# Optimization experiments

Measured on AMD Instinct MI355X. Metric: run time of the kernel, lower is better.

## Reference

```python
import jax, jax.numpy as jnp
import numpy as np

N, E, IN, H, C, G = 50000, 1600000, 128, 4, 32, 64  # nodes, edges, in_ch, heads, hidden, graphs
OUT = 1
NEG_SLOPE = 0.2


def setup_inputs() -> dict:
    key = jax.random.key(0)
    ks = jax.random.split(key, 16)
    d = {
        "x": jax.random.normal(ks[0], (N, IN), dtype=jnp.float32),
        "edge_index": jax.random.randint(ks[1], (2, E), 0, N, dtype=jnp.int64),
        "batch": jnp.sort(jax.random.randint(ks[2], (N,), 0, G, dtype=jnp.int64)),
    }
    s = 1.0 / np.sqrt(IN)
    # layer 0: in=IN, layer 1: in=H*C (=128)
    d["W0"] = jax.random.normal(ks[3], (IN, H * C), dtype=jnp.float32) * s
    d["a_src0"] = jax.random.normal(ks[4], (H, C), dtype=jnp.float32) * s
    d["a_dst0"] = jax.random.normal(ks[5], (H, C), dtype=jnp.float32) * s
    d["b0"] = jnp.zeros((H * C,), dtype=jnp.float32)
    d["W1"] = jax.random.normal(ks[6], (H * C, H * C), dtype=jnp.float32) * s
    d["a_src1"] = jax.random.normal(ks[7], (H, C), dtype=jnp.float32) * s
    d["a_dst1"] = jax.random.normal(ks[8], (H, C), dtype=jnp.float32) * s
    d["b1"] = jnp.zeros((H * C,), dtype=jnp.float32)
    d["lin_w"] = jax.random.normal(ks[9], (H * C, OUT), dtype=jnp.float32) * s
    d["lin_b"] = jnp.zeros((OUT,), dtype=jnp.float32)
    return d


def gat_conv(x, src, dst, W, a_src, a_dst, b):
    # x: [N, F_in]; src/dst: [E'] (self-loops already appended, PyG default)
    n = x.shape[0]
    xw = (x @ W).reshape(n, H, C)                      # [N, H, C]
    alpha_s = jnp.sum(xw * a_src, axis=-1)             # [N, H]
    alpha_d = jnp.sum(xw * a_dst, axis=-1)             # [N, H]
    e = jax.nn.leaky_relu(alpha_s[src] + alpha_d[dst], NEG_SLOPE)  # [E', H]
    # segment softmax over edges grouped by destination node
    m = jax.ops.segment_max(e, dst, num_segments=n)    # [N, H]
    ex = jnp.exp(e - m[dst])
    denom = jax.ops.segment_sum(ex, dst, num_segments=n)
    alpha = ex / denom[dst]                            # [E', H]
    msg = xw[src] * alpha[:, :, None]                  # [E', H, C]
    out = jax.ops.segment_sum(msg, dst, num_segments=n)
    return out.reshape(n, H * C) + b


def reference(x, edge_index, batch, W0, a_src0, a_dst0, b0, W1, a_src1, a_dst1, b1, lin_w, lin_b):
    loop = jnp.arange(N, dtype=edge_index.dtype)
    src = jnp.concatenate([edge_index[0], loop])
    dst = jnp.concatenate([edge_index[1], loop])
    h = gat_conv(x.astype(jnp.float32), src, dst, W0, a_src0, a_dst0, b0)
    h = jax.nn.elu(h)  # dropout is identity in eval mode
    h = gat_conv(h, src, dst, W1, a_src1, a_dst1, b1)
    h = jax.nn.elu(h)
    # global_mean_pool
    sums = jax.ops.segment_sum(h, batch, num_segments=G)          # [G, H*C]
    cnts = jax.ops.segment_sum(jnp.ones((N,), h.dtype), batch, num_segments=G)
    pooled = sums / jnp.maximum(cnts, 1.0)[:, None]
    return (pooled @ lin_w + lin_b).squeeze()                     # [G]
```

## Files before the change

kernel.cpp:

```cpp
#include <hip/hip_runtime.h>
#include <hip/hip_bf16.h>

#define NN 50000
#define EE 1600000
#define NEDGE (EE + NN)
#define HH 4
#define HC 128
#define GG 64
#define GMT 64
#define NBKT 196
#define BCAP 12544
#define BKE 2048
#define NB1 ((EE + BKE - 1) / BKE)

__device__ __forceinline__ float lrelu(float x) { return fmaxf(x, 0.2f * x); }

__device__ __forceinline__ unsigned packbf2(float a, float b) {
    unsigned ua = __float_as_uint(a);
    ua = (ua + 0x7fffu + ((ua >> 16) & 1u)) >> 16;
    unsigned ub = __float_as_uint(b);
    ub = (ub + 0x7fffu + ((ub >> 16) & 1u)) >> 16;
    return ua | (ub << 16);
}

__global__ __launch_bounds__(256) void binit(int* __restrict__ bcur) {
    int t = blockIdx.x * 256 + threadIdx.x;
    if (t < NBKT) bcur[t] = t * BCAP;
}

__global__ __launch_bounds__(256) void bucketize(const int* __restrict__ ei,
                                                 int* __restrict__ bcur,
                                                 uint2* __restrict__ pairs) {
    __shared__ int cnt[NBKT], off[NBKT], gbase[NBKT];
    __shared__ int wsum[4], woff[4];
    __shared__ uint2 stage[BKE];
    int t = threadIdx.x;
    int e0 = blockIdx.x * BKE;
    int n = EE - e0; if (n > BKE) n = BKE;
    for (int i = t; i < NBKT; i += 256) cnt[i] = 0;
    __syncthreads();
    unsigned dv[8], sv[8];
    int rk[8];
#pragma unroll
    for (int k = 0; k < 8; ++k) {
        int i = t + k * 256;
        if (i < n) {
            dv[k] = (unsigned)ei[EE + e0 + i];
            sv[k] = (unsigned)ei[e0 + i];
            rk[k] = atomicAdd(&cnt[dv[k] >> 8], 1);
        }
    }
    __syncthreads();
    {
        int v = (t < NBKT) ? cnt[t] : 0;
        int lane = t & 63, wv = t >> 6;
        int x = v;
#pragma unroll
        for (int o = 1; o < 64; o <<= 1) { int y = __shfl_up(x, o); if (lane >= o) x += y; }
        if (lane == 63) wsum[wv] = x;
        __syncthreads();
        if (t == 0) { int r = 0; for (int k2 = 0; k2 < 4; ++k2) { woff[k2] = r; r += wsum[k2]; } }
        __syncthreads();
        if (t < NBKT) off[t] = x - v + woff[wv];
    }
    __syncthreads();
#pragma unroll
    for (int k = 0; k < 8; ++k) {
        int i = t + k * 256;
        if (i < n) stage[off[dv[k] >> 8] + rk[k]] = make_uint2(dv[k], sv[k]);
    }
    __syncthreads();
    if (t < NBKT) { int c = cnt[t]; gbase[t] = c ? atomicAdd(&bcur[t], c) : 0; }
    __syncthreads();
    for (int i = t; i < n; i += 256) {
        uint2 pr = stage[i];
        int b = (int)(pr.x >> 8);
        pairs[(size_t)gbase[b] + (i - off[b])] = pr;
    }
}

__global__ __launch_bounds__(256) void bscan(const int* __restrict__ bcur,
                                             int* __restrict__ bbase) {
    int t = threadIdx.x;
    int v = 0;
    if (t < NBKT) {
        int pcnt = bcur[t] - t * BCAP;
        int nodes = NN - t * 256; if (nodes > 256) nodes = 256;
        v = pcnt + nodes;
    }
    int lane = t & 63, wv = t >> 6;
    int x = v;
#pragma unroll
    for (int o = 1; o < 64; o <<= 1) { int y = __shfl_up(x, o); if (lane >= o) x += y; }
    __shared__ int wsum[4], woff[4];
    if (lane == 63) wsum[wv] = x;
    __syncthreads();
    if (t == 0) { int r = 0; for (int k = 0; k < 4; ++k) { woff[k] = r; r += wsum[k]; } }
    __syncthreads();
    if (t < NBKT) bbase[t] = x - v + woff[wv];
}

__global__ __launch_bounds__(512) void debucket(const uint2* __restrict__ pairs,
                                                const int* __restrict__ bcur,
                                                const int* __restrict__ bbase,
                                                int* __restrict__ row_start,
                                                int* __restrict__ esrc) {
    __shared__ int cnt[256], off[256], cur[256];
    __shared__ int wsum[4], woff[4];
    __shared__ int stage[BCAP + 256];
    int b = blockIdx.x, t = threadIdx.x;
    int n0 = b * 256;
    int nnode = NN - n0; if (nnode > 256) nnode = 256;
    int pcnt = bcur[b] - b * BCAP;
    int base = bbase[b];
    if (t < 256) cnt[t] = 0;
    __syncthreads();
    for (int i = t; i < pcnt; i += 512)
        atomicAdd(&cnt[pairs[(size_t)b * BCAP + i].x & 255u], 1);
    __syncthreads();
    {
        int v = 0, x = 0;
        int lane = t & 63, wv = t >> 6;
        if (t < 256) {
            v = cnt[t] + (t < nnode ? 1 : 0);
            x = v;
#pragma unroll
            for (int o = 1; o < 64; o <<= 1) { int y = __shfl_up(x, o); if (lane >= o) x += y; }
            if (lane == 63) wsum[wv] = x;
        }
        __syncthreads();
        if (t == 0) { int r = 0; for (int k = 0; k < 4; ++k) { woff[k] = r; r += wsum[k]; } }
        __syncthreads();
        if (t < 256) off[t] = x - v + woff[wv];
    }
    __syncthreads();
    if (t < nnode) {
        int o = off[t];
        stage[o] = n0 + t;
        cur[t] = o + 1;
        row_start[n0 + t] = base + o;
    }
    __syncthreads();
    for (int i = t; i < pcnt; i += 512) {
        uint2 pr = pairs[(size_t)b * BCAP + i];
        int p = atomicAdd(&cur[pr.x & 255u], 1);
        stage[p] = (int)pr.y;
    }
    __syncthreads();
    int tot = pcnt + nnode;
    for (int i = t; i < tot; i += 512) esrc[base + i] = stage[i];
    if (b == NBKT - 1 && t == 0) row_start[NN] = NEDGE;
}

__global__ __launch_bounds__(256) void gemm_alpha(
    const float* __restrict__ X, const float* __restrict__ W,
    const float* __restrict__ a_src, const float* __restrict__ a_dst,
    unsigned* __restrict__ xwb, float* __restrict__ as_, float* __restrict__ ad_) {
    __shared__ float xs[GMT][HC + 4];
    int tid = threadIdx.x;
    int n0 = blockIdx.x * GMT;
    for (int i = tid; i < GMT * (HC / 4); i += 256) {
        int r = i >> 5, c4 = i & 31;
        int n = n0 + r;
        float4 v = (n < NN) ? ((const float4*)X)[(size_t)n * 32 + c4]
                            : make_float4(0.f, 0.f, 0.f, 0.f);
        *(float4*)&xs[r][c4 * 4] = v;
    }
    __syncthreads();

    int jg = tid & 31;
    int ng = tid >> 5;
    float4 acc[8] = {};
    for (int k = 0; k < HC; k += 4) {
        float4 wr[4];
#pragma unroll
        for (int dk = 0; dk < 4; ++dk) wr[dk] = ((const float4*)W)[(k + dk) * 32 + jg];
#pragma unroll
        for (int r = 0; r < 8; ++r) {
            float4 xv = *(const float4*)&xs[ng * 8 + r][k];
            acc[r].x = fmaf(xv.x, wr[0].x, acc[r].x);
            acc[r].y = fmaf(xv.x, wr[0].y, acc[r].y);
            acc[r].z = fmaf(xv.x, wr[0].z, acc[r].z);
            acc[r].w = fmaf(xv.x, wr[0].w, acc[r].w);
            acc[r].x = fmaf(xv.y, wr[1].x, acc[r].x);
            acc[r].y = fmaf(xv.y, wr[1].y, acc[r].y);
            acc[r].z = fmaf(xv.y, wr[1].z, acc[r].z);
            acc[r].w = fmaf(xv.y, wr[1].w, acc[r].w);
            acc[r].x = fmaf(xv.z, wr[2].x, acc[r].x);
            acc[r].y = fmaf(xv.z, wr[2].y, acc[r].y);
            acc[r].z = fmaf(xv.z, wr[2].z, acc[r].z);
            acc[r].w = fmaf(xv.z, wr[2].w, acc[r].w);
            acc[r].x = fmaf(xv.w, wr[3].x, acc[r].x);
            acc[r].y = fmaf(xv.w, wr[3].y, acc[r].y);
            acc[r].z = fmaf(xv.w, wr[3].z, acc[r].z);
            acc[r].w = fmaf(xv.w, wr[3].w, acc[r].w);
        }
    }
    float4 asv = ((const float4*)a_src)[jg];
    float4 adv = ((const float4*)a_dst)[jg];
#pragma unroll
    for (int r = 0; r < 8; ++r) {
        int n = n0 + ng * 8 + r;
        float ps = acc[r].x * asv.x + acc[r].y * asv.y + acc[r].z * asv.z + acc[r].w * asv.w;
        float pd = acc[r].x * adv.x + acc[r].y * adv.y + acc[r].z * adv.z + acc[r].w * adv.w;
        ps += __shfl_xor(ps, 1); pd += __shfl_xor(pd, 1);
        ps += __shfl_xor(ps, 2); pd += __shfl_xor(pd, 2);
        ps += __shfl_xor(ps, 4); pd += __shfl_xor(pd, 4);
        if (n < NN) {
            ((uint2*)xwb)[(size_t)n * 32 + jg] =
                make_uint2(packbf2(acc[r].x, acc[r].y), packbf2(acc[r].z, acc[r].w));
            if ((jg & 7) == 0) {
                int h = jg >> 3;
                as_[n * HH + h] = ps;
                ad_[n * HH + h] = pd;
            }
        }
    }
}

#define SWSTR 66
__global__ __launch_bounds__(256) void aggregate(
    const int* __restrict__ esrc, const int* __restrict__ row_start,
    const float* __restrict__ as_, const float* __restrict__ ad_,
    const unsigned* __restrict__ xwb, const float* __restrict__ bias,
    float* __restrict__ out) {
    __shared__ float2 sw_all[4][4 * SWSTR];
    int wid = (int)(threadIdx.x >> 6);
    int node = blockIdx.x * 4 + wid;
    if (node >= NN) return;
    int lane = threadIdx.x & 63;
    float2* sw = &sw_all[wid][0];
    int beg = row_start[node];
    int end = row_start[node + 1];
    float4 ad = ((const float4*)ad_)[node];

    int sub = lane >> 4;
    int c8 = lane & 15;
    int h = c8 >> 2;
    const char* xwp = (const char*)xwb + (c8 << 4);
    const char* asp = (const char*)as_;
    float4 accA = make_float4(0.f, 0.f, 0.f, 0.f);
    float4 accB = make_float4(0.f, 0.f, 0.f, 0.f);
    float dloc = 0.f;

    for (int base = beg; base < end; base += 64) {
        int i = base + lane;
        int cnt = end - base; if (cnt > 64) cnt = 64;
        if (i < end) {
            int s = esrc[i];
            float4 av = *(const float4*)(asp + ((unsigned)s << 4));
            float w0 = __expf(lrelu(av.x + ad.x));
            float w1 = __expf(lrelu(av.y + ad.y));
            float w2 = __expf(lrelu(av.z + ad.z));
            float w3 = __expf(lrelu(av.w + ad.w));
            float sf = __int_as_float(s);
            sw[0 * SWSTR + lane] = make_float2(sf, w0);
            sw[1 * SWSTR + lane] = make_float2(sf, w1);
            sw[2 * SWSTR + lane] = make_float2(sf, w2);
            sw[3 * SWSTR + lane] = make_float2(sf, w3);
        }
        int iters = (cnt + 3) >> 2;
        bool ok = sub < cnt;
        float2 sv = sw[h * SWSTR + (ok ? sub : 0)];
        float wj = ok ? sv.y : 0.f;
        unsigned row = ok ? ((unsigned)__float_as_int(sv.x) << 8) : 0u;
        uint4 v = *(const uint4*)(xwp + row);
        for (int it = 1; it <= iters; ++it) {
            int j1 = (it << 2) + sub;
            bool ok1 = j1 < cnt;
            float2 sv1 = sw[h * SWSTR + (ok1 ? j1 : 0)];
            float w1 = ok1 ? sv1.y : 0.f;
            unsigned row1 = ok1 ? ((unsigned)__float_as_int(sv1.x) << 8) : 0u;
            uint4 v1 = *(const uint4*)(xwp + row1);
            dloc += wj;
            accA.x = fmaf(wj, __uint_as_float(v.x << 16), accA.x);
            accA.y = fmaf(wj, __uint_as_float(v.x & 0xffff0000u), accA.y);
            accA.z = fmaf(wj, __uint_as_float(v.y << 16), accA.z);
            accA.w = fmaf(wj, __uint_as_float(v.y & 0xffff0000u), accA.w);
            accB.x = fmaf(wj, __uint_as_float(v.z << 16), accB.x);
            accB.y = fmaf(wj, __uint_as_float(v.z & 0xffff0000u), accB.y);
            accB.z = fmaf(wj, __uint_as_float(v.w << 16), accB.z);
            accB.w = fmaf(wj, __uint_as_float(v.w & 0xffff0000u), accB.w);
            v = v1; wj = w1;
        }
    }
#pragma unroll
    for (int off = 16; off <= 32; off <<= 1) {
        accA.x += __shfl_xor(accA.x, off);
        accA.y += __shfl_xor(accA.y, off);
        accA.z += __shfl_xor(accA.z, off);
        accA.w += __shfl_xor(accA.w, off);
        accB.x += __shfl_xor(accB.x, off);
        accB.y += __shfl_xor(accB.y, off);
        accB.z += __shfl_xor(accB.z, off);
        accB.w += __shfl_xor(accB.w, off);
        dloc += __shfl_xor(dloc, off);
    }
    if (sub == 0) {
        float inv = 1.f / dloc;
        float4 bb0 = ((const float4*)bias)[c8 * 2];
        float4 bb1 = ((const float4*)bias)[c8 * 2 + 1];
        float4 oA, oB;
        oA.x = fmaf(accA.x, inv, bb0.x);
        oA.y = fmaf(accA.y, inv, bb0.y);
        oA.z = fmaf(accA.z, inv, bb0.z);
        oA.w = fmaf(accA.w, inv, bb0.w);
        oB.x = fmaf(accB.x, inv, bb1.x);
        oB.y = fmaf(accB.y, inv, bb1.y);
        oB.z = fmaf(accB.z, inv, bb1.z);
        oB.w = fmaf(accB.w, inv, bb1.w);
        oA.x = oA.x > 0.f ? oA.x : expm1f(oA.x);
        oA.y = oA.y > 0.f ? oA.y : expm1f(oA.y);
        oA.z = oA.z > 0.f ? oA.z : expm1f(oA.z);
        oA.w = oA.w > 0.f ? oA.w : expm1f(oA.w);
        oB.x = oB.x > 0.f ? oB.x : expm1f(oB.x);
        oB.y = oB.y > 0.f ? oB.y : expm1f(oB.y);
        oB.z = oB.z > 0.f ? oB.z : expm1f(oB.z);
        oB.w = oB.w > 0.f ? oB.w : expm1f(oB.w);
        ((float4*)out)[(size_t)node * 32 + c8 * 2] = oA;
        ((float4*)out)[(size_t)node * 32 + c8 * 2 + 1] = oB;
    }
}

__global__ __launch_bounds__(128) void pool(
    const float* __restrict__ h1, const int* __restrict__ batch,
    float* __restrict__ sums, float* __restrict__ cnts) {
    int j = threadIdx.x;
    int n0 = blockIdx.x * 64;
    int n1 = n0 + 64; if (n1 > NN) n1 = NN;
    if (n0 >= NN) return;
    int cur = batch[n0];
    float local = 0.f;
    int cnt = 0;
    for (int n = n0; n < n1; ++n) {
        int g = batch[n];
        if (g != cur) {
            atomicAdd(&sums[cur * HC + j], local);
            if (j == 0) atomicAdd(&cnts[cur], (float)cnt);
            local = 0.f; cnt = 0; cur = g;
        }
        local += h1[(size_t)n * HC + j];
        ++cnt;
    }
    atomicAdd(&sums[cur * HC + j], local);
    if (j == 0) atomicAdd(&cnts[cur], (float)cnt);
}

__global__ __launch_bounds__(128) void head_out(
    const float* __restrict__ sums, const float* __restrict__ cnts,
    const float* __restrict__ lin_w, const float* __restrict__ lin_b,
    float* __restrict__ out) {
    int g = blockIdx.x;
    int j = threadIdx.x;
    float c = cnts[g];
    c = c > 1.f ? c : 1.f;
    float v = sums[g * HC + j] / c * lin_w[j];
    __shared__ float red[HC];
    red[j] = v;
    __syncthreads();
    for (int off = 64; off > 0; off >>= 1) {
        if (j < off) red[j] += red[j + off];
        __syncthreads();
    }
    if (j == 0) out[g] = red[0] + lin_b[0];
}

extern "C" void kernel_launch(void* const* d_in, const int* in_sizes, int n_in,
                              void* d_out, int out_size, void* d_ws, size_t ws_size,
                              hipStream_t stream) {
    const float* x   = (const float*)d_in[0];
    const int*   ei  = (const int*)d_in[1];
    const int*   bat = (const int*)d_in[2];
    const float* W0  = (const float*)d_in[3];
    const float* as0 = (const float*)d_in[4];
    const float* ad0 = (const float*)d_in[5];
    const float* b0  = (const float*)d_in[6];
    const float* W1  = (const float*)d_in[7];
    const float* as1 = (const float*)d_in[8];
    const float* ad1 = (const float*)d_in[9];
    const float* b1  = (const float*)d_in[10];
    const float* lw  = (const float*)d_in[11];
    const float* lb  = (const float*)d_in[12];
    float* out = (float*)d_out;

    char* w = (char*)d_ws;
    unsigned* xwb = (unsigned*)w; w += (size_t)NN * HC * 2;
    float* h0  = (float*)w;  w += (size_t)NN * HC * 4;
    float* as_ = (float*)w;  w += (size_t)NN * HH * 4;
    float* ad_ = (float*)w;  w += (size_t)NN * HH * 4;
    int* row_start = (int*)w; w += (size_t)(NN + 1) * 4;
    int* bcur      = (int*)w; w += (size_t)NBKT * 4;
    int* bbase     = (int*)w; w += (size_t)NBKT * 4;
    int* esrc      = (int*)w; w += (size_t)NEDGE * 4;
    uint2* pairs   = (uint2*)w; w += (size_t)NBKT * BCAP * 8;
    float* sums = (float*)w; w += (size_t)GG * HC * 4;
    float* cnts = (float*)w; w += (size_t)GG * 4;

    const int gb = (NN + GMT - 1) / GMT;
    const int ab = (NN + 3) / 4;

    binit<<<1, 256, 0, stream>>>(bcur);
    bucketize<<<NB1, 256, 0, stream>>>(ei, bcur, pairs);
    bscan<<<1, 256, 0, stream>>>(bcur, bbase);
    debucket<<<NBKT, 512, 0, stream>>>(pairs, bcur, bbase, row_start, esrc);

    gemm_alpha<<<gb, 256, 0, stream>>>(x, W0, as0, ad0, xwb, as_, ad_);
    aggregate<<<ab, 256, 0, stream>>>(esrc, row_start, as_, ad_, xwb, b0, h0);

    gemm_alpha<<<gb, 256, 0, stream>>>(h0, W1, as1, ad1, xwb, as_, ad_);
    aggregate<<<ab, 256, 0, stream>>>(esrc, row_start, as_, ad_, xwb, b1, h0);

    hipMemsetAsync(sums, 0, ((size_t)GG * HC + GG) * 4, stream);
    pool<<<(NN + 63) / 64, 128, 0, stream>>>(h0, bat, sums, cnts);
    head_out<<<GG, 128, 0, stream>>>(sums, cnts, lw, lb, out);
}
```

Before: 261.9 us.

## Fuse layer-0 GEMM with edge bucketize and fold bucket scan into debucket

Merges the layer-0 feature GEMM and edge bucketization into one launch. Even blocks do the GEMM and odd blocks bucketize edges, sharing LDS through a union, so compute-bound and memory-bound work run concurrently. The separate bscan kernel is removed: each debucket block now computes its own base offset by reducing the counts of all earlier buckets. This cuts launch count and serialization, at the cost of a larger LDS footprint per block and some redundant prefix work in every debucket block.

```diff
diff --git a/kernel.cpp b/kernel.cpp
--- a/kernel.cpp
+++ b/kernel.cpp
@@ -12,6 +12,7 @@
 #define BCAP 12544
 #define BKE 2048
 #define NB1 ((EE + BKE - 1) / BKE)
+#define GB ((NN + GMT - 1) / GMT)
 
 __device__ __forceinline__ float lrelu(float x) { return fmaxf(x, 0.2f * x); }
 
@@ -28,91 +29,157 @@
     if (t < NBKT) bcur[t] = t * BCAP;
 }
 
-__global__ __launch_bounds__(256) void bucketize(const int* __restrict__ ei,
-                                                 int* __restrict__ bcur,
-                                                 uint2* __restrict__ pairs) {
-    __shared__ int cnt[NBKT], off[NBKT], gbase[NBKT];
-    __shared__ int wsum[4], woff[4];
-    __shared__ uint2 stage[BKE];
+__global__ __launch_bounds__(256) void g0bkt(
+    const float* __restrict__ X, const float* __restrict__ W,
+    const float* __restrict__ a_src, const float* __restrict__ a_dst,
+    unsigned* __restrict__ xwb, float* __restrict__ as_, float* __restrict__ ad_,
+    const int* __restrict__ ei, int* __restrict__ bcur, uint2* __restrict__ pairs) {
+    __shared__ union U {
+        float xs[GMT][HC + 4];
+        struct {
+            int cnt[NBKT], off[NBKT], gbase[NBKT];
+            int wsum[4], woff[4];
+            uint2 stage[BKE];
+        } b;
+    } u;
     int t = threadIdx.x;
-    int e0 = blockIdx.x * BKE;
-    int n = EE - e0; if (n > BKE) n = BKE;
-    for (int i = t; i < NBKT; i += 256) cnt[i] = 0;
-    __syncthreads();
-    unsigned dv[8], sv[8];
-    int rk[8];
-#pragma unroll
-    for (int k = 0; k < 8; ++k) {
-        int i = t + k * 256;
-        if (i < n) {
-            dv[k] = (unsigned)ei[EE + e0 + i];
-            sv[k] = (unsigned)ei[e0 + i];
-            rk[k] = atomicAdd(&cnt[dv[k] >> 8], 1);
-        }
-    }
-    __syncthreads();
-    {
-        int v = (t < NBKT) ? cnt[t] : 0;
-        int lane = t & 63, wv = t >> 6;
-        int x = v;
-#pragma unroll
-        for (int o = 1; o < 64; o <<= 1) { int y = __shfl_up(x, o); if (lane >= o) x += y; }
-        if (lane == 63) wsum[wv] = x;
-        __syncthreads();
-        if (t == 0) { int r = 0; for (int k2 = 0; k2 < 4; ++k2) { woff[k2] = r; r += wsum[k2]; } }
-        __syncthreads();
-        if (t < NBKT) off[t] = x - v + woff[wv];
-    }
-    __syncthreads();
-#pragma unroll
-    for (int k = 0; k < 8; ++k) {
-        int i = t + k * 256;
-        if (i < n) stage[off[dv[k] >> 8] + rk[k]] = make_uint2(dv[k], sv[k]);
-    }
-    __syncthreads();
-    if (t < NBKT) { int c = cnt[t]; gbase[t] = c ? atomicAdd(&bcur[t], c) : 0; }
-    __syncthreads();
-    for (int i = t; i < n; i += 256) {
-        uint2 pr = stage[i];
-        int b = (int)(pr.x >> 8);
-        pairs[(size_t)gbase[b] + (i - off[b])] = pr;
-    }
-}
-
-__global__ __launch_bounds__(256) void bscan(const int* __restrict__ bcur,
-                                             int* __restrict__ bbase) {
-    int t = threadIdx.x;
-    int v = 0;
-    if (t < NBKT) {
-        int pcnt = bcur[t] - t * BCAP;
-        int nodes = NN - t * 256; if (nodes > 256) nodes = 256;
-        v = pcnt + nodes;
-    }
-    int lane = t & 63, wv = t >> 6;
-    int x = v;
-#pragma unroll
-    for (int o = 1; o < 64; o <<= 1) { int y = __shfl_up(x, o); if (lane >= o) x += y; }
-    __shared__ int wsum[4], woff[4];
-    if (lane == 63) wsum[wv] = x;
-    __syncthreads();
-    if (t == 0) { int r = 0; for (int k = 0; k < 4; ++k) { woff[k] = r; r += wsum[k]; } }
-    __syncthreads();
-    if (t < NBKT) bbase[t] = x - v + woff[wv];
+    int id = (int)(blockIdx.x >> 1);
+
+    if ((blockIdx.x & 1) == 0) {
+        int n0 = id * GMT;
+        for (int i = t; i < GMT * (HC / 4); i += 256) {
+            int r = i >> 5, c4 = i & 31;
+            int n = n0 + r;
+            float4 v = (n < NN) ? ((const float4*)X)[(size_t)n * 32 + c4]
+                                : make_float4(0.f, 0.f, 0.f, 0.f);
+            *(float4*)&u.xs[r][c4 * 4] = v;
+        }
+        __syncthreads();
+        int jg = t & 31;
+        int ng = t >> 5;
+        float4 acc[8] = {};
+        for (int k = 0; k < HC; k += 4) {
+            float4 wr[4];
+#pragma unroll
+            for (int dk = 0; dk < 4; ++dk) wr[dk] = ((const float4*)W)[(k + dk) * 32 + jg];
+#pragma unroll
+            for (int r = 0; r < 8; ++r) {
+                float4 xv = *(const float4*)&u.xs[ng * 8 + r][k];
+                acc[r].x = fmaf(xv.x, wr[0].x, acc[r].x);
+                acc[r].y = fmaf(xv.x, wr[0].y, acc[r].y);
+                acc[r].z = fmaf(xv.x, wr[0].z, acc[r].z);
+                acc[r].w = fmaf(xv.x, wr[0].w, acc[r].w);
+                acc[r].x = fmaf(xv.y, wr[1].x, acc[r].x);
+                acc[r].y = fmaf(xv.y, wr[1].y, acc[r].y);
+                acc[r].z = fmaf(xv.y, wr[1].z, acc[r].z);
+                acc[r].w = fmaf(xv.y, wr[1].w, acc[r].w);
+                acc[r].x = fmaf(xv.z, wr[2].x, acc[r].x);
+                acc[r].y = fmaf(xv.z, wr[2].y, acc[r].y);
+                acc[r].z = fmaf(xv.z, wr[2].z, acc[r].z);
+                acc[r].w = fmaf(xv.z, wr[2].w, acc[r].w);
+                acc[r].x = fmaf(xv.w, wr[3].x, acc[r].x);
+                acc[r].y = fmaf(xv.w, wr[3].y, acc[r].y);
+                acc[r].z = fmaf(xv.w, wr[3].z, acc[r].z);
+                acc[r].w = fmaf(xv.w, wr[3].w, acc[r].w);
+            }
+        }
+        float4 asv = ((const float4*)a_src)[jg];
+        float4 adv = ((const float4*)a_dst)[jg];
+#pragma unroll
+        for (int r = 0; r < 8; ++r) {
+            int n = n0 + ng * 8 + r;
+            float ps = acc[r].x * asv.x + acc[r].y * asv.y + acc[r].z * asv.z + acc[r].w * asv.w;
+            float pd = acc[r].x * adv.x + acc[r].y * adv.y + acc[r].z * adv.z + acc[r].w * adv.w;
+            ps += __shfl_xor(ps, 1); pd += __shfl_xor(pd, 1);
+            ps += __shfl_xor(ps, 2); pd += __shfl_xor(pd, 2);
+            ps += __shfl_xor(ps, 4); pd += __shfl_xor(pd, 4);
+            if (n < NN) {
+                ((uint2*)xwb)[(size_t)n * 32 + jg] =
+                    make_uint2(packbf2(acc[r].x, acc[r].y), packbf2(acc[r].z, acc[r].w));
+                if ((jg & 7) == 0) {
+                    int h = jg >> 3;
+                    as_[n * HH + h] = ps;
+                    ad_[n * HH + h] = pd;
+                }
+            }
+        }
+    } else {
+        int e0 = id * BKE;
+        int n = EE - e0; if (n > BKE) n = BKE;
+        for (int i = t; i < NBKT; i += 256) u.b.cnt[i] = 0;
+        __syncthreads();
+        unsigned dv[8], sv[8];
+        int rk[8];
+#pragma unroll
+        for (int k = 0; k < 8; ++k) {
+            int i = t + k * 256;
+            if (i < n) {
+                dv[k] = (unsigned)ei[EE + e0 + i];
+                sv[k] = (unsigned)ei[e0 + i];
+                rk[k] = atomicAdd(&u.b.cnt[dv[k] >> 8], 1);
+            }
+        }
+        __syncthreads();
+        {
+            int v = (t < NBKT) ? u.b.cnt[t] : 0;
+            int lane = t & 63, wv = t >> 6;
+            int x = v;
+#pragma unroll
+            for (int o = 1; o < 64; o <<= 1) { int y = __shfl_up(x, o); if (lane >= o) x += y; }
+            if (lane == 63) u.b.wsum[wv] = x;
+            __syncthreads();
+            if (t == 0) { int r = 0; for (int k2 = 0; k2 < 4; ++k2) { u.b.woff[k2] = r; r += u.b.wsum[k2]; } }
+            __syncthreads();
+            if (t < NBKT) u.b.off[t] = x - v + u.b.woff[wv];
+        }
+        __syncthreads();
+#pragma unroll
+        for (int k = 0; k < 8; ++k) {
+            int i = t + k * 256;
+            if (i < n) u.b.stage[u.b.off[dv[k] >> 8] + rk[k]] = make_uint2(dv[k], sv[k]);
+        }
+        __syncthreads();
+        if (t < NBKT) { int c = u.b.cnt[t]; u.b.gbase[t] = c ? atomicAdd(&bcur[t], c) : 0; }
+        __syncthreads();
+        for (int i = t; i < n; i += 256) {
+            uint2 pr = u.b.stage[i];
+            int b = (int)(pr.x >> 8);
+            pairs[(size_t)u.b.gbase[b] + (i - u.b.off[b])] = pr;
+        }
+    }
 }
 
 __global__ __launch_bounds__(512) void debucket(const uint2* __restrict__ pairs,
                                                 const int* __restrict__ bcur,
-                                                const int* __restrict__ bbase,
                                                 int* __restrict__ row_start,
                                                 int* __restrict__ esrc) {
     __shared__ int cnt[256], off[256], cur[256];
     __shared__ int wsum[4], woff[4];
+    __shared__ int wred[8];
     __shared__ int stage[BCAP + 256];
     int b = blockIdx.x, t = threadIdx.x;
     int n0 = b * 256;
     int nnode = NN - n0; if (nnode > 256) nnode = 256;
     int pcnt = bcur[b] - b * BCAP;
-    int base = bbase[b];
+
+    int base;
+    {
+        int v = 0;
+        if (t < b) {
+            int pc = bcur[t] - t * BCAP;
+            int nd = (t < NBKT - 1) ? 256 : (NN - (NBKT - 1) * 256);
+            v = pc + nd;
+        }
+        int lane = t & 63, wv = t >> 6;
+#pragma unroll
+        for (int o = 1; o < 64; o <<= 1) v += __shfl_xor(v, o);
+        if (lane == 0) wred[wv] = v;
+        __syncthreads();
+        if (t == 0) { int s = 0; for (int k = 0; k < 8; ++k) s += wred[k]; wred[0] = s; }
+        __syncthreads();
+        base = wred[0];
+    }
+    __syncthreads();
     if (t < 256) cnt[t] = 0;
     __syncthreads();
     for (int i = t; i < pcnt; i += 512)
@@ -390,24 +457,21 @@
     float* ad_ = (float*)w;  w += (size_t)NN * HH * 4;
     int* row_start = (int*)w; w += (size_t)(NN + 1) * 4;
     int* bcur      = (int*)w; w += (size_t)NBKT * 4;
-    int* bbase     = (int*)w; w += (size_t)NBKT * 4;
     int* esrc      = (int*)w; w += (size_t)NEDGE * 4;
     uint2* pairs   = (uint2*)w; w += (size_t)NBKT * BCAP * 8;
     float* sums = (float*)w; w += (size_t)GG * HC * 4;
     float* cnts = (float*)w; w += (size_t)GG * 4;
 
-    const int gb = (NN + GMT - 1) / GMT;
     const int ab = (NN + 3) / 4;
 
     binit<<<1, 256, 0, stream>>>(bcur);
-    bucketize<<<NB1, 256, 0, stream>>>(ei, bcur, pairs);
-    bscan<<<1, 256, 0, stream>>>(bcur, bbase);
-    debucket<<<NBKT, 512, 0, stream>>>(pairs, bcur, bbase, row_start, esrc);
-
-    gemm_alpha<<<gb, 256, 0, stream>>>(x, W0, as0, ad0, xwb, as_, ad_);
+    g0bkt<<<GB + NB1, 256, 0, stream>>>(x, W0, as0, ad0, xwb, as_, ad_,
+                                        ei, bcur, pairs);
+    debucket<<<NBKT, 512, 0, stream>>>(pairs, bcur, row_start, esrc);
+
     aggregate<<<ab, 256, 0, stream>>>(esrc, row_start, as_, ad_, xwb, b0, h0);
 
-    gemm_alpha<<<gb, 256, 0, stream>>>(h0, W1, as1, ad1, xwb, as_, ad_);
+    gemm_alpha<<<GB, 256, 0, stream>>>(h0, W1, as1, ad1, xwb, as_, ad_);
     aggregate<<<ab, 256, 0, stream>>>(esrc, row_start, as_, ad_, xwb, b1, h0);
 
     hipMemsetAsync(sums, 0, ((size_t)GG * HC + GG) * 4, stream);
```

After: 249.3 us. -4.8%, faster.
